# Kernel optimization log

Measured on AMD Instinct MI355X. Metric: run time of the kernel, lower is better.

## Reference

```python
import jax, jax.numpy as jnp
import numpy as np

B, N, K, C, CM = 4, 1024, 9, 32, 128
SIGMA = 1.0
EPS = 1e-5
SLOPE = 0.01  # LeakyReLU default negative slope


def _batchnorm(x, gamma, beta):
    # training-mode BatchNorm1d over the point dimension
    m = x.mean(axis=0)
    v = x.var(axis=0)
    return gamma * (x - m) * jax.lax.rsqrt(v + EPS) + beta


def setup_inputs() -> dict:
    key = jax.random.key(0)
    ks = jax.random.split(key, 8)
    positions = jax.random.uniform(ks[0], (B * N, 2), jnp.float32) * 10.0
    weights = jax.random.normal(ks[1], (B * N, C), jnp.float32)
    # learned kernel offsets (grid-init in original; random offsets of same scale here)
    kernel_pos = jax.random.normal(ks[2], (K, 2), jnp.float32) * (2.0 * SIGMA)
    conv_w = jax.random.normal(ks[3], (K, C, C), jnp.float32) / np.sqrt(K * C)
    w1 = jax.random.normal(ks[4], (C, CM), jnp.float32) / np.sqrt(C)
    w2 = jax.random.normal(ks[5], (CM, C), jnp.float32) / np.sqrt(CM)
    return {
        "positions": positions,
        "weights": weights,
        "kernel_pos": kernel_pos,
        "conv_w": conv_w,
        "bn_gamma": jnp.ones((C,), jnp.float32),
        "bn_beta": jnp.zeros((C,), jnp.float32),
        "w1": w1,
        "b1": jnp.zeros((CM,), jnp.float32),
        "bn1_gamma": jnp.ones((CM,), jnp.float32),
        "bn1_beta": jnp.zeros((CM,), jnp.float32),
        "w2": w2,
        "b2": jnp.zeros((C,), jnp.float32),
        "n_batch": B,
        "n_points": N,
    }


def reference(positions, weights, kernel_pos, conv_w, bn_gamma, bn_beta,
              w1, b1, bn1_gamma, bn1_beta, w2, b2, n_batch, n_points):
    b, n = n_batch, n_points
    k = kernel_pos.shape[0]
    c = weights.shape[-1]
    pos = positions.reshape(b, n, 2)
    w = weights.reshape(b, n, c)

    # KernelConv: each component spawns K shifted components with channel mixing
    comp_pos = pos[:, :, None, :] + kernel_pos[None, None, :, :]      # [b,n,k,2]
    comp_w = jnp.einsum('bnc,kcd->bnkd', w, conv_w)                   # [b,n,k,c]

    # KernelSample: evaluate the resulting Gaussian mixture at the input positions
    diff = pos[:, :, None, None, :] - comp_pos[:, None, :, :, :]      # [b,i,n,k,2]
    dist2 = jnp.sum(diff * diff, axis=-1)                             # [b,i,n,k]
    kmat = jnp.exp(-dist2 / (2.0 * SIGMA * SIGMA))
    y = jnp.einsum('bink,bnkc->bic', kmat, comp_w)                    # [b,i,c]
    y = jax.nn.leaky_relu(y, SLOPE)
    y = y.reshape(b * n, c)

    # conv_norm + residual add of input weights
    y = _batchnorm(y, bn_gamma, bn_beta)
    y = y + weights

    # PyG MLP [C, CM, C], act_first=True, plain_last=True
    h = y @ w1 + b1
    h = jax.nn.leaky_relu(h, SLOPE)
    h = _batchnorm(h, bn1_gamma, bn1_beta)
    delta = h @ w2 + b2

    return y + delta  # output weights [b*n, c]; positions pass through unchanged
```

## Files before the change

### kernel.cpp

```cpp
#include <hip/hip_runtime.h>

#define BB 4
#define NN 1024
#define KK 9
#define C  32
#define CM 128
#define M  (BB*NN)
#define EPSB 1e-5f
#define SLOPE 0.01f

#define SCH 4
#define NCH 256
#define NSUB 32
#define KDIM 288
#define KPAD 296
#define CHUNK_F16 (32*KPAD)

typedef _Float16 f16x8 __attribute__((ext_vector_type(8)));
typedef _Float16 f16x4 __attribute__((ext_vector_type(4)));
typedef float    f32x4 __attribute__((ext_vector_type(4)));

__device__ __forceinline__ float leaky(float x){ return x > 0.f ? x : SLOPE*x; }

__global__ __launch_bounds__(256) void k1_compw(const float* __restrict__ w,
                                                const float* __restrict__ conv_w,
                                                _Float16* __restrict__ cwh,
                                                float* __restrict__ stats){
  __shared__ float cwl[3*C*C];
  int bid = blockIdx.x;
  int kt  = bid % 3;
  int sub = (bid/3)&7, nc = (bid/24)&3, b = bid/96;
  int tid = threadIdx.x;
  if (bid == 0){ for (int i = tid; i < 320; i += 256) stats[i] = 0.f; }

  const float4* cs = (const float4*)(conv_w + kt*3*C*C);
  float4* cd = (float4*)cwl;
  for (int v = tid; v < 768; v += 256) cd[v] = cs[v];

  int nl = tid & 31, dq = tid >> 5;
  int row = ((b*4 + nc)*8 + sub)*32 + nl;
  float wreg[32];
  const float4* wr = (const float4*)(w + (size_t)row*C);
  #pragma unroll
  for (int j = 0; j < 8; ++j){
    float4 t = wr[j];
    wreg[4*j]=t.x; wreg[4*j+1]=t.y; wreg[4*j+2]=t.z; wreg[4*j+3]=t.w;
  }
  __syncthreads();

  _Float16* outb = cwh + (size_t)((b*4+nc)*8 + sub)*CHUNK_F16;
  const float4* cv = (const float4*)cwl;
  #pragma unroll
  for (int kl = 0; kl < 3; ++kl){
    float a0=0.f, a1=0.f, a2=0.f, a3=0.f;
    #pragma unroll
    for (int c = 0; c < C; ++c){
      float4 t = cv[kl*256 + c*8 + dq];
      a0 += wreg[c]*t.x; a1 += wreg[c]*t.y; a2 += wreg[c]*t.z; a3 += wreg[c]*t.w;
    }
    int k = kt*3 + kl;
    outb[(dq*4+0)*KPAD + k*32 + nl] = (_Float16)a0;
    outb[(dq*4+1)*KPAD + k*32 + nl] = (_Float16)a1;
    outb[(dq*4+2)*KPAD + k*32 + nl] = (_Float16)a2;
    outb[(dq*4+3)*KPAD + k*32 + nl] = (_Float16)a3;
  }
}

__global__ __launch_bounds__(256) void k2_main(const float* __restrict__ pos,
                                               const float* __restrict__ kpos,
                                               const _Float16* __restrict__ cwh,
                                               float* __restrict__ part){
  __shared__ _Float16 km[32*KPAD];
  __shared__ _Float16 cw[32*KPAD];
  __shared__ float pnl[NCH*2];
  int bid = blockIdx.x;
  int nc = bid & 3, it = (bid>>2)&31, b = bid>>7;
  int tid = threadIdx.x;
  int lane = tid & 63, wid = tid >> 6;
  int i0 = (wid>>1)*16, c0 = (wid&1)*16;
  int mm = lane & 15, quad = lane >> 4;

  const float* pbase = pos + (size_t)(b*NN + nc*NCH)*2;
  for (int v = tid; v < NCH*2; v += 256) pnl[v] = pbase[v];

  int ig = tid >> 3, np = tid & 7;
  float pix = pos[(size_t)(b*NN + it*32 + ig)*2];
  float piy = pos[(size_t)(b*NN + it*32 + ig)*2 + 1];
  float kx[KK], ky[KK];
  #pragma unroll
  for (int k = 0; k < KK; ++k){ kx[k] = kpos[2*k]; ky[k] = kpos[2*k+1]; }

  f32x4 acc = {0.f,0.f,0.f,0.f};
  __syncthreads();

  for (int s = 0; s < 8; ++s){
    const float4* srcs = (const float4*)(cwh + (size_t)((b*4+nc)*8 + s)*CHUNK_F16);
    float4* dst = (float4*)cw;
    for (int v = tid; v < CHUNK_F16/8; v += 256) dst[v] = srcs[v];

    float dx[4], dy[4];
    #pragma unroll
    for (int jj = 0; jj < 4; ++jj){
      int nl = np*4 + jj;
      dx[jj] = pix - pnl[2*(s*32+nl)];
      dy[jj] = piy - pnl[2*(s*32+nl)+1];
    }
    #pragma unroll
    for (int k = 0; k < KK; ++k){
      f16x4 ev;
      #pragma unroll
      for (int jj = 0; jj < 4; ++jj){
        float ddx = dx[jj]-kx[k], ddy = dy[jj]-ky[k];
        ev[jj] = (_Float16)__expf(-0.5f*(ddx*ddx + ddy*ddy));
      }
      *(f16x4*)&km[ig*KPAD + k*32 + np*4] = ev;
    }
    __syncthreads();

    #pragma unroll
    for (int ks = 0; ks < 9; ++ks){
      f16x8 a  = *(const f16x8*)&km[(i0+mm)*KPAD + ks*32 + quad*8];
      f16x8 bf = *(const f16x8*)&cw[(c0+mm)*KPAD + ks*32 + quad*8];
      acc = __builtin_amdgcn_mfma_f32_16x16x32_f16(a, bf, acc, 0, 0, 0);
    }
    __syncthreads();
  }

  int grow0 = b*NN + it*32 + i0;
  #pragma unroll
  for (int r = 0; r < 4; ++r){
    int grow = grow0 + quad*4 + r;
    part[((size_t)nc*M + grow)*C + c0 + mm] = acc[r];
  }
}

__global__ __launch_bounds__(256) void k3_reduce(const float* __restrict__ part,
                                                 float* __restrict__ z,
                                                 float* __restrict__ stats,
                                                 int S){
  __shared__ float ls1[C], ls2[C];
  int tid = threadIdx.x;
  if (tid < C){ ls1[tid]=0.f; ls2[tid]=0.f; }
  __syncthreads();
  size_t idx = (size_t)blockIdx.x*256 + tid;
  float s = 0.f;
  for (int p = 0; p < S; ++p) s += part[(size_t)p*M*C + idx];
  s = leaky(s);
  z[idx] = s;
  atomicAdd(&ls1[tid & (C-1)], s);
  atomicAdd(&ls2[tid & (C-1)], s*s);
  __syncthreads();
  if (tid < C){ atomicAdd(&stats[tid], ls1[tid]); atomicAdd(&stats[C+tid], ls2[tid]); }
}

__global__ __launch_bounds__(256) void k4_mlp1(const float* __restrict__ z,
                                               const float* __restrict__ weights,
                                               const float* __restrict__ bn_g,
                                               const float* __restrict__ bn_b,
                                               const float* __restrict__ w1,
                                               const float* __restrict__ b1,
                                               float* __restrict__ stats,
                                               float* __restrict__ y,
                                               float* __restrict__ h){
  __shared__ float w1l[C*CM];
  __shared__ float yl[16*C];
  __shared__ float lt1[CM], lt2[CM];
  int tid = threadIdx.x;
  int row0 = blockIdx.x * 16;
  for (int i = tid; i < C*CM; i += 256) w1l[i] = w1[i];
  if (tid < CM){ lt1[tid]=0.f; lt2[tid]=0.f; }
  #pragma unroll
  for (int j = 0; j < 2; ++j){
    int e = tid + j*256;
    int c  = e & (C-1);
    int rl = e >> 5;
    float s1 = stats[c], s2 = stats[C + c];
    float mean = s1 * (1.f/M);
    float var  = s2 * (1.f/M) - mean*mean;
    float sc = bn_g[c] * rsqrtf(var + EPSB);
    float sh = bn_b[c] - mean*sc;
    int row = row0 + rl;
    float v = z[(size_t)row*C + c]*sc + sh + weights[(size_t)row*C + c];
    yl[e] = v;
    y[(size_t)row*C + c] = v;
  }
  __syncthreads();
  #pragma unroll
  for (int j = 0; j < 8; ++j){
    int e = tid + j*256;
    int col = e & (CM-1);
    int rl  = e >> 7;
    float acc = b1[col];
    #pragma unroll
    for (int c = 0; c < C; ++c) acc += yl[rl*C + c] * w1l[c*CM + col];
    acc = leaky(acc);
    h[(size_t)(row0+rl)*CM + col] = acc;
    atomicAdd(&lt1[col], acc);
    atomicAdd(&lt2[col], acc*acc);
  }
  __syncthreads();
  if (tid < CM){
    atomicAdd(&stats[2*C + tid],      lt1[tid]);
    atomicAdd(&stats[2*C + CM + tid], lt2[tid]);
  }
}

__global__ __launch_bounds__(256) void k5_mlp2(const float* __restrict__ h,
                                               const float* __restrict__ y,
                                               const float* __restrict__ bn1_g,
                                               const float* __restrict__ bn1_b,
                                               const float* __restrict__ w2,
                                               const float* __restrict__ b2,
                                               const float* __restrict__ stats,
                                               float* __restrict__ out){
  __shared__ float w2l[CM*C];
  __shared__ float hl[16*CM];
  int tid = threadIdx.x;
  int row0 = blockIdx.x * 16;
  for (int i = tid; i < CM*C; i += 256) w2l[i] = w2[i];
  #pragma unroll
  for (int j = 0; j < 8; ++j){
    int e = tid + j*256;
    int col = e & (CM-1);
    int rl  = e >> 7;
    float t1 = stats[2*C + col], t2 = stats[2*C + CM + col];
    float mean = t1*(1.f/M);
    float var  = t2*(1.f/M) - mean*mean;
    float sc = bn1_g[col]*rsqrtf(var + EPSB);
    float sh = bn1_b[col] - mean*sc;
    hl[e] = h[(size_t)(row0+rl)*CM + col]*sc + sh;
  }
  __syncthreads();
  #pragma unroll
  for (int j = 0; j < 2; ++j){
    int e = tid + j*256;
    int c  = e & (C-1);
    int rl = e >> 5;
    float acc = b2[c];
    #pragma unroll
    for (int jj = 0; jj < CM; ++jj) acc += hl[rl*CM + jj] * w2l[jj*C + c];
    int row = row0 + rl;
    out[(size_t)row*C + c] = y[(size_t)row*C + c] + acc;
  }
}

extern "C" void kernel_launch(void* const* d_in, const int* in_sizes, int n_in,
                              void* d_out, int out_size, void* d_ws, size_t ws_size,
                              hipStream_t stream) {
  const float* positions = (const float*)d_in[0];
  const float* weights   = (const float*)d_in[1];
  const float* kpos      = (const float*)d_in[2];
  const float* conv_w    = (const float*)d_in[3];
  const float* bn_g      = (const float*)d_in[4];
  const float* bn_b      = (const float*)d_in[5];
  const float* w1        = (const float*)d_in[6];
  const float* b1        = (const float*)d_in[7];
  const float* bn1_g     = (const float*)d_in[8];
  const float* bn1_b     = (const float*)d_in[9];
  const float* w2        = (const float*)d_in[10];
  const float* b2        = (const float*)d_in[11];
  float* out = (float*)d_out;

  float* ws = (float*)d_ws;
  size_t off = 0;
  _Float16* cwh = (_Float16*)(ws + off); off += (size_t)128*CHUNK_F16/2;
  float* part  = ws + off; off += (size_t)SCH*M*C;
  float* z     = ws + off; off += (size_t)M*C;
  float* y     = ws + off; off += (size_t)M*C;
  float* h     = ws + off; off += (size_t)M*CM;
  float* stats = ws + off; off += 320;

  k1_compw<<<384, 256, 0, stream>>>(weights, conv_w, cwh, stats);
  k2_main <<<512, 256, 0, stream>>>(positions, kpos, cwh, part);
  k3_reduce<<<(M*C)/256, 256, 0, stream>>>(part, z, stats, SCH);
  k4_mlp1<<<M/16, 256, 0, stream>>>(z, weights, bn_g, bn_b, w1, b1, stats, y, h);
  k5_mlp2<<<M/16, 256, 0, stream>>>(h, y, bn1_g, bn1_b, w2, b2, stats, out);
}
```

Baseline: 146.9 us.

## Fuse five kernels into one persistent kernel with software grid barriers

Merges the compw, main MFMA, reduce, and two MLP kernels into a single 512-block launch, with atomic-counter grid barriers separating the phases and shared memory reused across them. The aim is to remove the launch gaps between five small kernels. In exchange it adds a memset launch, spin-wait barrier cost, and a deadlock risk if all 512 blocks are not co-resident. It also leaves some blocks idle in phases that use fewer blocks.

```diff
diff --git a/kernel.cpp b/kernel.cpp
--- a/kernel.cpp
+++ b/kernel.cpp
@@ -9,10 +9,9 @@
 #define EPSB 1e-5f
 #define SLOPE 0.01f
 
+#define GRID_BLOCKS 512
 #define SCH 4
 #define NCH 256
-#define NSUB 32
-#define KDIM 288
 #define KPAD 296
 #define CHUNK_F16 (32*KPAD)
 
@@ -22,225 +21,236 @@
 
 __device__ __forceinline__ float leaky(float x){ return x > 0.f ? x : SLOPE*x; }
 
-__global__ __launch_bounds__(256) void k1_compw(const float* __restrict__ w,
-                                                const float* __restrict__ conv_w,
-                                                _Float16* __restrict__ cwh,
-                                                float* __restrict__ stats){
-  __shared__ float cwl[3*C*C];
+__device__ __forceinline__ void gridbar(int* cnt){
+  __syncthreads();
+  if (threadIdx.x == 0){
+    __threadfence();
+    __hip_atomic_fetch_add(cnt, 1, __ATOMIC_ACQ_REL, __HIP_MEMORY_SCOPE_AGENT);
+    while (__hip_atomic_load(cnt, __ATOMIC_ACQUIRE, __HIP_MEMORY_SCOPE_AGENT) < GRID_BLOCKS){
+      __builtin_amdgcn_s_sleep(2);
+    }
+  }
+  __syncthreads();
+}
+
+__global__ __launch_bounds__(256, 2) void fused_all(
+    const float* __restrict__ pos,
+    const float* __restrict__ weights,
+    const float* __restrict__ kpos,
+    const float* __restrict__ conv_w,
+    const float* __restrict__ bn_g,  const float* __restrict__ bn_b,
+    const float* __restrict__ w1,    const float* __restrict__ b1,
+    const float* __restrict__ bn1_g, const float* __restrict__ bn1_b,
+    const float* __restrict__ w2,    const float* __restrict__ b2,
+    float* __restrict__ out,
+    _Float16* __restrict__ cwh,
+    float* __restrict__ part,
+    float* __restrict__ z,
+    float* __restrict__ y,
+    float* __restrict__ h,
+    float* __restrict__ stats,
+    int* __restrict__ bar)
+{
+  __shared__ __align__(16) char smem[40960];
   int bid = blockIdx.x;
-  int kt  = bid % 3;
-  int sub = (bid/3)&7, nc = (bid/24)&3, b = bid/96;
   int tid = threadIdx.x;
+
   if (bid == 0){ for (int i = tid; i < 320; i += 256) stats[i] = 0.f; }
-
-  const float4* cs = (const float4*)(conv_w + kt*3*C*C);
-  float4* cd = (float4*)cwl;
-  for (int v = tid; v < 768; v += 256) cd[v] = cs[v];
-
-  int nl = tid & 31, dq = tid >> 5;
-  int row = ((b*4 + nc)*8 + sub)*32 + nl;
-  float wreg[32];
-  const float4* wr = (const float4*)(w + (size_t)row*C);
-  #pragma unroll
-  for (int j = 0; j < 8; ++j){
-    float4 t = wr[j];
-    wreg[4*j]=t.x; wreg[4*j+1]=t.y; wreg[4*j+2]=t.z; wreg[4*j+3]=t.w;
-  }
-  __syncthreads();
-
-  _Float16* outb = cwh + (size_t)((b*4+nc)*8 + sub)*CHUNK_F16;
-  const float4* cv = (const float4*)cwl;
-  #pragma unroll
-  for (int kl = 0; kl < 3; ++kl){
-    float a0=0.f, a1=0.f, a2=0.f, a3=0.f;
-    #pragma unroll
-    for (int c = 0; c < C; ++c){
-      float4 t = cv[kl*256 + c*8 + dq];
-      a0 += wreg[c]*t.x; a1 += wreg[c]*t.y; a2 += wreg[c]*t.z; a3 += wreg[c]*t.w;
-    }
-    int k = kt*3 + kl;
-    outb[(dq*4+0)*KPAD + k*32 + nl] = (_Float16)a0;
-    outb[(dq*4+1)*KPAD + k*32 + nl] = (_Float16)a1;
-    outb[(dq*4+2)*KPAD + k*32 + nl] = (_Float16)a2;
-    outb[(dq*4+3)*KPAD + k*32 + nl] = (_Float16)a3;
-  }
-}
-
-__global__ __launch_bounds__(256) void k2_main(const float* __restrict__ pos,
-                                               const float* __restrict__ kpos,
-                                               const _Float16* __restrict__ cwh,
-                                               float* __restrict__ part){
-  __shared__ _Float16 km[32*KPAD];
-  __shared__ _Float16 cw[32*KPAD];
-  __shared__ float pnl[NCH*2];
-  int bid = blockIdx.x;
-  int nc = bid & 3, it = (bid>>2)&31, b = bid>>7;
-  int tid = threadIdx.x;
-  int lane = tid & 63, wid = tid >> 6;
-  int i0 = (wid>>1)*16, c0 = (wid&1)*16;
-  int mm = lane & 15, quad = lane >> 4;
-
-  const float* pbase = pos + (size_t)(b*NN + nc*NCH)*2;
-  for (int v = tid; v < NCH*2; v += 256) pnl[v] = pbase[v];
-
-  int ig = tid >> 3, np = tid & 7;
-  float pix = pos[(size_t)(b*NN + it*32 + ig)*2];
-  float piy = pos[(size_t)(b*NN + it*32 + ig)*2 + 1];
-  float kx[KK], ky[KK];
-  #pragma unroll
-  for (int k = 0; k < KK; ++k){ kx[k] = kpos[2*k]; ky[k] = kpos[2*k+1]; }
-
-  f32x4 acc = {0.f,0.f,0.f,0.f};
-  __syncthreads();
-
-  for (int s = 0; s < 8; ++s){
-    const float4* srcs = (const float4*)(cwh + (size_t)((b*4+nc)*8 + s)*CHUNK_F16);
-    float4* dst = (float4*)cw;
-    for (int v = tid; v < CHUNK_F16/8; v += 256) dst[v] = srcs[v];
-
-    float dx[4], dy[4];
-    #pragma unroll
-    for (int jj = 0; jj < 4; ++jj){
-      int nl = np*4 + jj;
-      dx[jj] = pix - pnl[2*(s*32+nl)];
-      dy[jj] = piy - pnl[2*(s*32+nl)+1];
-    }
-    #pragma unroll
-    for (int k = 0; k < KK; ++k){
-      f16x4 ev;
+  if (bid < 384){
+    float* cwl = (float*)smem;
+    int kt  = bid % 3;
+    int sub = (bid/3)&7, nc = (bid/24)&3, b = bid/96;
+
+    const float4* cs = (const float4*)(conv_w + kt*3*C*C);
+    float4* cd = (float4*)cwl;
+    for (int v = tid; v < 768; v += 256) cd[v] = cs[v];
+
+    int nl = tid & 31, dq = tid >> 5;
+    int row = ((b*4 + nc)*8 + sub)*32 + nl;
+    float wreg[32];
+    const float4* wr = (const float4*)(weights + (size_t)row*C);
+    #pragma unroll
+    for (int j = 0; j < 8; ++j){
+      float4 t = wr[j];
+      wreg[4*j]=t.x; wreg[4*j+1]=t.y; wreg[4*j+2]=t.z; wreg[4*j+3]=t.w;
+    }
+    __syncthreads();
+
+    _Float16* outb = cwh + (size_t)((b*4+nc)*8 + sub)*CHUNK_F16;
+    const float4* cv = (const float4*)cwl;
+    #pragma unroll
+    for (int kl = 0; kl < 3; ++kl){
+      float a0=0.f, a1=0.f, a2=0.f, a3=0.f;
+      #pragma unroll
+      for (int c = 0; c < C; ++c){
+        float4 t = cv[kl*256 + c*8 + dq];
+        a0 += wreg[c]*t.x; a1 += wreg[c]*t.y; a2 += wreg[c]*t.z; a3 += wreg[c]*t.w;
+      }
+      int k = kt*3 + kl;
+      outb[(dq*4+0)*KPAD + k*32 + nl] = (_Float16)a0;
+      outb[(dq*4+1)*KPAD + k*32 + nl] = (_Float16)a1;
+      outb[(dq*4+2)*KPAD + k*32 + nl] = (_Float16)a2;
+      outb[(dq*4+3)*KPAD + k*32 + nl] = (_Float16)a3;
+    }
+  }
+  gridbar(&bar[0]);
+
+  {
+    _Float16* km = (_Float16*)smem;
+    _Float16* cw = (_Float16*)(smem + 18944);
+    float* pnl   = (float*)(smem + 37888);
+    int nc = bid & 3, it = (bid>>2)&31, b = bid>>7;
+    int lane = tid & 63, wid = tid >> 6;
+    int i0 = (wid>>1)*16, c0 = (wid&1)*16;
+    int mm = lane & 15, quad = lane >> 4;
+
+    const float* pbase = pos + (size_t)(b*NN + nc*NCH)*2;
+    for (int v = tid; v < NCH*2; v += 256) pnl[v] = pbase[v];
+
+    int ig = tid >> 3, np = tid & 7;
+    float pix = pos[(size_t)(b*NN + it*32 + ig)*2];
+    float piy = pos[(size_t)(b*NN + it*32 + ig)*2 + 1];
+    float kx[KK], ky[KK];
+    #pragma unroll
+    for (int k = 0; k < KK; ++k){ kx[k] = kpos[2*k]; ky[k] = kpos[2*k+1]; }
+
+    f32x4 acc = {0.f,0.f,0.f,0.f};
+    __syncthreads();
+
+    for (int s = 0; s < 8; ++s){
+      const float4* srcs = (const float4*)(cwh + (size_t)((b*4+nc)*8 + s)*CHUNK_F16);
+      float4* dst = (float4*)cw;
+      for (int v = tid; v < CHUNK_F16/8; v += 256) dst[v] = srcs[v];
+
+      float dx[4], dy[4];
       #pragma unroll
       for (int jj = 0; jj < 4; ++jj){
-        float ddx = dx[jj]-kx[k], ddy = dy[jj]-ky[k];
-        ev[jj] = (_Float16)__expf(-0.5f*(ddx*ddx + ddy*ddy));
-      }
-      *(f16x4*)&km[ig*KPAD + k*32 + np*4] = ev;
-    }
-    __syncthreads();
-
-    #pragma unroll
-    for (int ks = 0; ks < 9; ++ks){
-      f16x8 a  = *(const f16x8*)&km[(i0+mm)*KPAD + ks*32 + quad*8];
-      f16x8 bf = *(const f16x8*)&cw[(c0+mm)*KPAD + ks*32 + quad*8];
-      acc = __builtin_amdgcn_mfma_f32_16x16x32_f16(a, bf, acc, 0, 0, 0);
-    }
-    __syncthreads();
-  }
-
-  int grow0 = b*NN + it*32 + i0;
-  #pragma unroll
-  for (int r = 0; r < 4; ++r){
-    int grow = grow0 + quad*4 + r;
-    part[((size_t)nc*M + grow)*C + c0 + mm] = acc[r];
-  }
-}
-
-__global__ __launch_bounds__(256) void k3_reduce(const float* __restrict__ part,
-                                                 float* __restrict__ z,
-                                                 float* __restrict__ stats,
-                                                 int S){
-  __shared__ float ls1[C], ls2[C];
-  int tid = threadIdx.x;
-  if (tid < C){ ls1[tid]=0.f; ls2[tid]=0.f; }
-  __syncthreads();
-  size_t idx = (size_t)blockIdx.x*256 + tid;
-  float s = 0.f;
-  for (int p = 0; p < S; ++p) s += part[(size_t)p*M*C + idx];
-  s = leaky(s);
-  z[idx] = s;
-  atomicAdd(&ls1[tid & (C-1)], s);
-  atomicAdd(&ls2[tid & (C-1)], s*s);
-  __syncthreads();
-  if (tid < C){ atomicAdd(&stats[tid], ls1[tid]); atomicAdd(&stats[C+tid], ls2[tid]); }
-}
-
-__global__ __launch_bounds__(256) void k4_mlp1(const float* __restrict__ z,
-                                               const float* __restrict__ weights,
-                                               const float* __restrict__ bn_g,
-                                               const float* __restrict__ bn_b,
-                                               const float* __restrict__ w1,
-                                               const float* __restrict__ b1,
-                                               float* __restrict__ stats,
-                                               float* __restrict__ y,
-                                               float* __restrict__ h){
-  __shared__ float w1l[C*CM];
-  __shared__ float yl[16*C];
-  __shared__ float lt1[CM], lt2[CM];
-  int tid = threadIdx.x;
-  int row0 = blockIdx.x * 16;
-  for (int i = tid; i < C*CM; i += 256) w1l[i] = w1[i];
-  if (tid < CM){ lt1[tid]=0.f; lt2[tid]=0.f; }
-  #pragma unroll
-  for (int j = 0; j < 2; ++j){
-    int e = tid + j*256;
-    int c  = e & (C-1);
-    int rl = e >> 5;
-    float s1 = stats[c], s2 = stats[C + c];
-    float mean = s1 * (1.f/M);
-    float var  = s2 * (1.f/M) - mean*mean;
-    float sc = bn_g[c] * rsqrtf(var + EPSB);
-    float sh = bn_b[c] - mean*sc;
-    int row = row0 + rl;
-    float v = z[(size_t)row*C + c]*sc + sh + weights[(size_t)row*C + c];
-    yl[e] = v;
-    y[(size_t)row*C + c] = v;
-  }
-  __syncthreads();
-  #pragma unroll
-  for (int j = 0; j < 8; ++j){
-    int e = tid + j*256;
-    int col = e & (CM-1);
-    int rl  = e >> 7;
-    float acc = b1[col];
-    #pragma unroll
-    for (int c = 0; c < C; ++c) acc += yl[rl*C + c] * w1l[c*CM + col];
-    acc = leaky(acc);
-    h[(size_t)(row0+rl)*CM + col] = acc;
-    atomicAdd(&lt1[col], acc);
-    atomicAdd(&lt2[col], acc*acc);
-  }
-  __syncthreads();
-  if (tid < CM){
-    atomicAdd(&stats[2*C + tid],      lt1[tid]);
-    atomicAdd(&stats[2*C + CM + tid], lt2[tid]);
-  }
-}
-
-__global__ __launch_bounds__(256) void k5_mlp2(const float* __restrict__ h,
-                                               const float* __restrict__ y,
-                                               const float* __restrict__ bn1_g,
-                                               const float* __restrict__ bn1_b,
-                                               const float* __restrict__ w2,
-                                               const float* __restrict__ b2,
-                                               const float* __restrict__ stats,
-                                               float* __restrict__ out){
-  __shared__ float w2l[CM*C];
-  __shared__ float hl[16*CM];
-  int tid = threadIdx.x;
-  int row0 = blockIdx.x * 16;
-  for (int i = tid; i < CM*C; i += 256) w2l[i] = w2[i];
-  #pragma unroll
-  for (int j = 0; j < 8; ++j){
-    int e = tid + j*256;
-    int col = e & (CM-1);
-    int rl  = e >> 7;
-    float t1 = stats[2*C + col], t2 = stats[2*C + CM + col];
-    float mean = t1*(1.f/M);
-    float var  = t2*(1.f/M) - mean*mean;
-    float sc = bn1_g[col]*rsqrtf(var + EPSB);
-    float sh = bn1_b[col] - mean*sc;
-    hl[e] = h[(size_t)(row0+rl)*CM + col]*sc + sh;
-  }
-  __syncthreads();
-  #pragma unroll
-  for (int j = 0; j < 2; ++j){
-    int e = tid + j*256;
-    int c  = e & (C-1);
-    int rl = e >> 5;
-    float acc = b2[c];
-    #pragma unroll
-    for (int jj = 0; jj < CM; ++jj) acc += hl[rl*CM + jj] * w2l[jj*C + c];
-    int row = row0 + rl;
-    out[(size_t)row*C + c] = y[(size_t)row*C + c] + acc;
+        int nl = np*4 + jj;
+        dx[jj] = pix - pnl[2*(s*32+nl)];
+        dy[jj] = piy - pnl[2*(s*32+nl)+1];
+      }
+      #pragma unroll
+      for (int k = 0; k < KK; ++k){
+        f16x4 ev;
+        #pragma unroll
+        for (int jj = 0; jj < 4; ++jj){
+          float ddx = dx[jj]-kx[k], ddy = dy[jj]-ky[k];
+          ev[jj] = (_Float16)__expf(-0.5f*(ddx*ddx + ddy*ddy));
+        }
+        *(f16x4*)&km[ig*KPAD + k*32 + np*4] = ev;
+      }
+      __syncthreads();
+
+      #pragma unroll
+      for (int ks = 0; ks < 9; ++ks){
+        f16x8 a  = *(const f16x8*)&km[(i0+mm)*KPAD + ks*32 + quad*8];
+        f16x8 bf = *(const f16x8*)&cw[(c0+mm)*KPAD + ks*32 + quad*8];
+        acc = __builtin_amdgcn_mfma_f32_16x16x32_f16(a, bf, acc, 0, 0, 0);
+      }
+      __syncthreads();
+    }
+
+    int grow0 = b*NN + it*32 + i0;
+    #pragma unroll
+    for (int r = 0; r < 4; ++r){
+      int grow = grow0 + quad*4 + r;
+      part[((size_t)nc*M + grow)*C + c0 + mm] = acc[r];
+    }
+  }
+  gridbar(&bar[1]);
+
+  {
+    float* ls1 = (float*)smem;
+    float* ls2 = ls1 + C;
+    if (tid < C){ ls1[tid]=0.f; ls2[tid]=0.f; }
+    __syncthreads();
+    size_t idx = (size_t)bid*256 + tid;
+    float s = 0.f;
+    #pragma unroll
+    for (int p = 0; p < SCH; ++p) s += part[(size_t)p*M*C + idx];
+    s = leaky(s);
+    z[idx] = s;
+    atomicAdd(&ls1[tid & (C-1)], s);
+    atomicAdd(&ls2[tid & (C-1)], s*s);
+    __syncthreads();
+    if (tid < C){ atomicAdd(&stats[tid], ls1[tid]); atomicAdd(&stats[C+tid], ls2[tid]); }
+  }
+  gridbar(&bar[2]);
+
+  if (bid < 256){
+    float* w1l = (float*)smem;
+    float* yl  = (float*)(smem + 16384);
+    float* lt1 = (float*)(smem + 18432);
+    float* lt2 = (float*)(smem + 18944);
+    int row0 = bid * 16;
+    for (int i = tid; i < C*CM; i += 256) w1l[i] = w1[i];
+    if (tid < CM){ lt1[tid]=0.f; lt2[tid]=0.f; }
+    #pragma unroll
+    for (int j = 0; j < 2; ++j){
+      int e = tid + j*256;
+      int c  = e & (C-1);
+      int rl = e >> 5;
+      float s1 = stats[c], s2 = stats[C + c];
+      float mean = s1 * (1.f/M);
+      float var  = s2 * (1.f/M) - mean*mean;
+      float sc = bn_g[c] * rsqrtf(var + EPSB);
+      float sh = bn_b[c] - mean*sc;
+      int row = row0 + rl;
+      float v = z[(size_t)row*C + c]*sc + sh + weights[(size_t)row*C + c];
+      yl[e] = v;
+      y[(size_t)row*C + c] = v;
+    }
+    __syncthreads();
+    #pragma unroll
+    for (int j = 0; j < 8; ++j){
+      int e = tid + j*256;
+      int col = e & (CM-1);
+      int rl  = e >> 7;
+      float acc = b1[col];
+      #pragma unroll
+      for (int c = 0; c < C; ++c) acc += yl[rl*C + c] * w1l[c*CM + col];
+      acc = leaky(acc);
+      h[(size_t)(row0+rl)*CM + col] = acc;
+      atomicAdd(&lt1[col], acc);
+      atomicAdd(&lt2[col], acc*acc);
+    }
+    __syncthreads();
+    if (tid < CM){
+      atomicAdd(&stats[2*C + tid],      lt1[tid]);
+      atomicAdd(&stats[2*C + CM + tid], lt2[tid]);
+    }
+  }
+  gridbar(&bar[3]);
+
+  if (bid < 256){
+    float* w2l = (float*)smem;
+    float* hl  = (float*)(smem + 16384);
+    int row0 = bid * 16;
+    for (int i = tid; i < CM*C; i += 256) w2l[i] = w2[i];
+    #pragma unroll
+    for (int j = 0; j < 8; ++j){
+      int e = tid + j*256;
+      int col = e & (CM-1);
+      int rl  = e >> 7;
+      float t1 = stats[2*C + col], t2 = stats[2*C + CM + col];
+      float mean = t1*(1.f/M);
+      float var  = t2*(1.f/M) - mean*mean;
+      float sc = bn1_g[col]*rsqrtf(var + EPSB);
+      float sh = bn1_b[col] - mean*sc;
+      hl[e] = h[(size_t)(row0+rl)*CM + col]*sc + sh;
+    }
+    __syncthreads();
+    #pragma unroll
+    for (int j = 0; j < 2; ++j){
+      int e = tid + j*256;
+      int c  = e & (C-1);
+      int rl = e >> 5;
+      float acc = b2[c];
+      #pragma unroll
+      for (int jj = 0; jj < CM; ++jj) acc += hl[rl*CM + jj] * w2l[jj*C + c];
+      int row = row0 + rl;
+      out[(size_t)row*C + c] = y[(size_t)row*C + c] + acc;
+    }
   }
 }
 
@@ -269,10 +279,10 @@
   float* y     = ws + off; off += (size_t)M*C;
   float* h     = ws + off; off += (size_t)M*CM;
   float* stats = ws + off; off += 320;
-
-  k1_compw<<<384, 256, 0, stream>>>(weights, conv_w, cwh, stats);
-  k2_main <<<512, 256, 0, stream>>>(positions, kpos, cwh, part);
-  k3_reduce<<<(M*C)/256, 256, 0, stream>>>(part, z, stats, SCH);
-  k4_mlp1<<<M/16, 256, 0, stream>>>(z, weights, bn_g, bn_b, w1, b1, stats, y, h);
-  k5_mlp2<<<M/16, 256, 0, stream>>>(h, y, bn1_g, bn1_b, w2, b2, stats, out);
+  int* bar     = (int*)(ws + off); off += 4;
+
+  hipMemsetAsync(bar, 0, 4*sizeof(int), stream);
+  fused_all<<<GRID_BLOCKS, 256, 0, stream>>>(
+      positions, weights, kpos, conv_w, bn_g, bn_b, w1, b1,
+      bn1_g, bn1_b, w2, b2, out, cwh, part, z, y, h, stats, bar);
 }
```

Measured after the change: 279.7 us. 90.4% more time.
